# Optimization experiments

Hardware: AMD Instinct MI355X
Metric: run time of the kernel (lower is better)

## Reference

```python
import jax, jax.numpy as jnp
import numpy as np
import math

C = 512          # in_planes
H = 8            # num_heads
D = C // H       # head_dim = 64
EPS = 1e-12      # torch F.normalize eps


def _l2norm(x):
    # F.normalize(x, dim=-1): x / max(||x||_2, eps)
    n = jnp.sqrt(jnp.sum(x * x, axis=-1, keepdims=True))
    return x / jnp.maximum(n, EPS)


def setup_inputs() -> dict:
    key = jax.random.key(0)
    ks = jax.random.split(key, 8)
    q = jax.random.normal(ks[0], (8, 8, 256, C), dtype=jnp.float32)
    kv = jax.random.normal(ks[1], (8, 8, 512, C), dtype=jnp.float32)
    s = 0.02
    Wq = jax.random.normal(ks[2], (C, C), dtype=jnp.float32) * s
    bq = jax.random.normal(ks[3], (C,), dtype=jnp.float32) * s
    Wkv = jax.random.normal(ks[4], (2 * C, C), dtype=jnp.float32) * s
    bkv = jax.random.normal(ks[5], (2 * C,), dtype=jnp.float32) * s
    Wm = jax.random.normal(ks[6], (C, C), dtype=jnp.float32) * s
    bm = jax.random.normal(ks[7], (C,), dtype=jnp.float32) * s
    return {"q": q, "kv": kv, "Wq": Wq, "bq": bq, "Wkv": Wkv, "bkv": bkv, "Wm": Wm, "bm": bm}


def reference(q, kv, Wq, bq, Wkv, bkv, Wm, bm):
    b, t, lq, c = q.shape
    lk = kv.shape[2]
    shortcut = q

    # Q projection -> (b,t,h,lq,d), L2-normalized over d
    qh = (q @ Wq.T + bq).reshape(b, t, lq, H, D)
    qh = _l2norm(jnp.moveaxis(qh, 3, 2))  # (b,t,h,lq,d)

    # KV projection -> (b,t,2h,lk,d); first H heads = k, last H = v
    kvh = (kv @ Wkv.T + bkv).reshape(b, t, lk, 2 * H, D)
    kvh = jnp.moveaxis(kvh, 3, 2)          # (b,t,2h,lk,d)
    kh = _l2norm(kvh[:, :, :H])            # (b,t,h,lk,d)
    vh = _l2norm(kvh[:, :, H:])            # (b,t,h,lk,d)

    # cosine attention
    att = jnp.einsum('bthqd,bthkd->bthqk', qh, kh) / math.sqrt(D)
    att = jax.nn.softmax(att, axis=-1)
    x = jnp.einsum('bthqk,bthkd->bthqd', att, vh)  # (b,t,h,lq,d)

    # merge heads, output projection, residual
    x = jnp.moveaxis(x, 2, 3).reshape(b, t, lq, c)
    return x @ Wm.T + bm + shortcut
```

## Files before the change

### kernel.cpp

```cpp
#include <hip/hip_runtime.h>
#include <hip/hip_bf16.h>

using bf = __bf16;
typedef __attribute__((ext_vector_type(8))) __bf16 bf16x8;
typedef __attribute__((ext_vector_type(4))) float f32x4;

#define MFMA(a, b, c) __builtin_amdgcn_mfma_f32_16x16x32_bf16((a), (b), (c), 0, 0, 0)
#define GLL16(g, s)                                                         \
    __builtin_amdgcn_global_load_lds(                                       \
        (const __attribute__((address_space(1))) void*)(g),                 \
        (__attribute__((address_space(3))) void*)(s), 16, 0, 0)

static __device__ __forceinline__ void cvt_one(const float* __restrict__ s,
                                               bf* __restrict__ d, int i)
{
    const f32x4 a = ((const f32x4*)s)[2 * i];
    const f32x4 b = ((const f32x4*)s)[2 * i + 1];
    bf16x8 r;
#pragma unroll
    for (int k = 0; k < 4; ++k) { r[k] = (bf)a[k]; r[4 + k] = (bf)b[k]; }
    ((bf16x8*)d)[i] = r;
}

__global__ __launch_bounds__(256) void cvt3(const float* __restrict__ s1, bf* __restrict__ d1, int n1,
                                            const float* __restrict__ s2, bf* __restrict__ d2, int n2,
                                            const float* __restrict__ s3, bf* __restrict__ d3, int n3)
{
    int i = blockIdx.x * 256 + threadIdx.x;
    if (i < n1) { cvt_one(s1, d1, i); return; }
    i -= n1;
    if (i < n2) { cvt_one(s2, d2, i); return; }
    i -= n2;
    if (i < n3) cvt_one(s3, d3, i);
}

template <int EPI, int GH, int LGR, int AF32>
__global__ __launch_bounds__(256) void gemm128(
    const void* __restrict__ Ap, const bf* __restrict__ W,
    const float* __restrict__ bias, const float* __restrict__ res,
    void* __restrict__ Cout, int M, int N, int K)
{
    __shared__ __attribute__((aligned(16))) bf As[128 * 32];
    __shared__ __attribute__((aligned(16))) bf Bs[128 * 32];

    const int lane = threadIdx.x & 63;
    const int wave = threadIdx.x >> 6;
    const int lm = lane & 15;
    const int quad = lane >> 4;
    const int row0 = blockIdx.x * 128, col0 = blockIdx.y * 128;
    const int wrow = (wave >> 1) * 64, wcol = (wave & 1) * 64;

    const int sr = lane >> 2;
    const int sc = (lane & 3) * 8;
    const bf* Ag = nullptr;
    const float* Agf = nullptr;
    if (AF32) Agf = (const float*)Ap + (size_t)(row0 + wave * 32 + sr) * K + sc;
    else      Ag  = (const bf*)Ap + (size_t)(row0 + wave * 32 + sr) * K + sc;
    const bf* Wg = W + (size_t)(col0 + wave * 32 + sr) * K + sc;
    bf* AsW = As + wave * 1024;
    bf* BsW = Bs + wave * 1024;

    f32x4 acc[4][4] = {};

    for (int k0 = 0; k0 < K; k0 += 32) {
        if (AF32) {
            f32x4 u0 = *(const f32x4*)(Agf + k0);
            f32x4 u1 = *(const f32x4*)(Agf + k0 + 4);
            f32x4 u2 = *(const f32x4*)(Agf + (size_t)16 * K + k0);
            f32x4 u3 = *(const f32x4*)(Agf + (size_t)16 * K + k0 + 4);
            bf16x8 r0, r1;
#pragma unroll
            for (int e = 0; e < 4; ++e) {
                r0[e] = (bf)u0[e]; r0[4 + e] = (bf)u1[e];
                r1[e] = (bf)u2[e]; r1[4 + e] = (bf)u3[e];
            }
            *(bf16x8*)(AsW + lane * 8) = r0;
            *(bf16x8*)(AsW + 512 + lane * 8) = r1;
        } else {
            GLL16(Ag + k0, AsW);
            GLL16(Ag + (size_t)16 * K + k0, AsW + 512);
        }
        GLL16(Wg + k0, BsW);
        GLL16(Wg + (size_t)16 * K + k0, BsW + 512);
        __syncthreads();

        bf16x8 a[4], b[4];
#pragma unroll
        for (int i = 0; i < 4; ++i)
            a[i] = *(const bf16x8*)(As + (wrow + i * 16 + lm) * 32 + quad * 8);
#pragma unroll
        for (int j = 0; j < 4; ++j)
            b[j] = *(const bf16x8*)(Bs + (wcol + j * 16 + lm) * 32 + quad * 8);
#pragma unroll
        for (int i = 0; i < 4; ++i)
#pragma unroll
            for (int j = 0; j < 4; ++j)
                acc[i][j] = MFMA(a[i], b[j], acc[i][j]);
        __syncthreads();
    }

    float bv[4];
#pragma unroll
    for (int j = 0; j < 4; ++j) bv[j] = bias[col0 + wcol + j * 16 + lm];

    if (EPI == 0) {
        bf* C = (bf*)Cout;
        const int g = (col0 + wcol) >> 6;
#pragma unroll
        for (int i = 0; i < 4; ++i) {
#pragma unroll
            for (int rg = 0; rg < 4; ++rg) {
                float v[4];
                float ss = 0.f;
#pragma unroll
                for (int j = 0; j < 4; ++j) {
                    const float x = acc[i][j][rg] + bv[j];
                    v[j] = x;
                    ss += x * x;
                }
                ss += __shfl_xor(ss, 1, 64);
                ss += __shfl_xor(ss, 2, 64);
                ss += __shfl_xor(ss, 4, 64);
                ss += __shfl_xor(ss, 8, 64);
                const float inv = 1.0f / fmaxf(sqrtf(ss), 1e-12f);
                const int row = row0 + wrow + i * 16 + quad * 4 + rg;
                const int bt = row >> LGR;
                const int rl = row & ((1 << LGR) - 1);
                bf* Cr = C + (((size_t)(bt * GH + g) << LGR) + rl) * 64;
#pragma unroll
                for (int j = 0; j < 4; ++j)
                    Cr[j * 16 + lm] = (bf)(v[j] * inv);
            }
        }
    } else {
        float* C = (float*)Cout;
#pragma unroll
        for (int i = 0; i < 4; ++i) {
#pragma unroll
            for (int rg = 0; rg < 4; ++rg) {
                const int row = row0 + wrow + i * 16 + quad * 4 + rg;
#pragma unroll
                for (int j = 0; j < 4; ++j) {
                    const size_t idx = (size_t)row * N + col0 + wcol + j * 16 + lm;
                    C[idx] = acc[i][j][rg] + bv[j] + res[idx];
                }
            }
        }
    }
}

template <int GH, int LGR>
__global__ __launch_bounds__(512, 2) void gemm256(
    const float* __restrict__ A, const bf* __restrict__ W,
    const float* __restrict__ bias, bf* __restrict__ C,
    int M, int N, int K)
{
    extern __shared__ __attribute__((aligned(16))) char smem[];
    char* Asm = smem;
    char* Bsm = smem + 65536;

    const int tid = threadIdx.x;
    const int lane = tid & 63;
    const int lm = lane & 15;
    const int quad = lane >> 4;
    const int wave = tid >> 6;
    const int wm = wave >> 2;
    const int wn = wave & 3;
    const int row0 = blockIdx.x * 256, col0 = blockIdx.y * 256;
    const int NT = K >> 6;

    const int trow = tid >> 3;
    const int slotL = tid & 7;
    const int sphys = slotL ^ (trow & 7);
    const int tslot = slotL ^ (trow & 7);
    const float* Af = A + (size_t)(row0 + trow) * K + slotL * 8;
    const bf* Wth = W + (size_t)(col0 + trow) * K + tslot * 8;

    const char* aBase = Asm + wm * 16384 + lm * 128;
    const char* bBase = Bsm + (wn >> 1) * 16384 + ((wn & 1) * 64 + lm) * 128;
    const int skz0 = ((quad ^ (lm & 7)) << 4);
    const int skz1 = (((4 + quad) ^ (lm & 7)) << 4);

    f32x4 acc[8][4] = {};
    f32x4 areg[4][2];

    auto ldA = [&](int kt) {
#pragma unroll
        for (int hs = 0; hs < 4; ++hs) {
            const float* p = Af + (size_t)((hs >> 1) * 128 + (hs & 1) * 64) * K + kt * 64;
            areg[hs][0] = ((const f32x4*)p)[0];
            areg[hs][1] = ((const f32x4*)p)[1];
        }
    };
    auto wrA = [&](int kt) {
        const int bo = (kt & 1) * 32768;
#pragma unroll
        for (int hs = 0; hs < 4; ++hs) {
            bf16x8 r;
#pragma unroll
            for (int e = 0; e < 4; ++e) {
                r[e] = (bf)areg[hs][0][e];
                r[4 + e] = (bf)areg[hs][1][e];
            }
            *(bf16x8*)(Asm + bo + (hs >> 1) * 16384 + (hs & 1) * 8192 + trow * 128 + sphys * 16) = r;
        }
    };
    auto stB = [&](int kt) {
        const int bo = (kt & 1) * 32768;
#pragma unroll
        for (int h = 0; h < 2; ++h)
#pragma unroll
            for (int s = 0; s < 2; ++s)
                GLL16(Wth + (size_t)(h * 128 + s * 64) * K + kt * 64,
                      Bsm + bo + h * 16384 + s * 8192 + tid * 16);
    };

#define LOADA(bo, mh, kk)                                                     \
    _Pragma("unroll")                                                         \
    for (int mm = 0; mm < 4; ++mm)                                            \
        a[mm] = *(const bf16x8*)(aBase + (bo) + ((mh) * 4 + mm) * 2048        \
                                 + ((kk) ? skz1 : skz0));
#define LOADB(bo, kk)                                                         \
    _Pragma("unroll")                                                         \
    for (int j = 0; j < 4; ++j)                                               \
        b[j] = *(const bf16x8*)(bBase + (bo) + j * 2048                       \
                                + ((kk) ? skz1 : skz0));
#define PH_OPEN()                                                             \
    __builtin_amdgcn_s_barrier();                                             \
    asm volatile("s_waitcnt lgkmcnt(0)" ::: "memory");                        \
    __builtin_amdgcn_s_setprio(1)
#define MM16(mh)                                                              \
    _Pragma("unroll")                                                         \
    for (int mm = 0; mm < 4; ++mm)                                            \
        _Pragma("unroll")                                                     \
        for (int j = 0; j < 4; ++j)                                           \
            acc[(mh) * 4 + mm][j] = MFMA(a[mm], b[j], acc[(mh) * 4 + mm][j]);
#define PH_CLOSE()                                                            \
    __builtin_amdgcn_s_setprio(0);                                            \
    __builtin_amdgcn_s_barrier()

    stB(0); ldA(0); stB(1);
    asm volatile("s_waitcnt vmcnt(4)" ::: "memory");
    wrA(0);
    asm volatile("s_waitcnt lgkmcnt(0)" ::: "memory");
    __builtin_amdgcn_s_barrier();

    for (int it = 0; it < NT; it += 2) {
        const int more = (it + 2 < NT);
        bf16x8 a[4], b[4];

        LOADA(0, 0, 0) LOADB(0, 0) ldA(it + 1);
        PH_OPEN(); MM16(0) PH_CLOSE();

        LOADA(0, 1, 0)
        PH_OPEN(); MM16(1) PH_CLOSE();

        LOADA(0, 0, 1) LOADB(0, 1)
        PH_OPEN(); MM16(0) PH_CLOSE();

        LOADA(0, 1, 1) if (more) stB(it + 2);
        PH_OPEN(); MM16(1)
        __builtin_amdgcn_s_setprio(0);
        if (more) { asm volatile("s_waitcnt vmcnt(4)" ::: "memory"); }
        else      { asm volatile("s_waitcnt vmcnt(0)" ::: "memory"); }
        wrA(it + 1);
        asm volatile("s_waitcnt lgkmcnt(0)" ::: "memory");
        __builtin_amdgcn_s_barrier();

        LOADA(32768, 0, 0) LOADB(32768, 0) if (more) ldA(it + 2);
        PH_OPEN(); MM16(0) PH_CLOSE();

        LOADA(32768, 1, 0)
        PH_OPEN(); MM16(1) PH_CLOSE();

        LOADA(32768, 0, 1) LOADB(32768, 1)
        PH_OPEN(); MM16(0) PH_CLOSE();

        LOADA(32768, 1, 1) if (more) stB(it + 3);
        PH_OPEN(); MM16(1)
        __builtin_amdgcn_s_setprio(0);
        if (more) {
            asm volatile("s_waitcnt vmcnt(4)" ::: "memory");
            wrA(it + 2);
            asm volatile("s_waitcnt lgkmcnt(0)" ::: "memory");
        }
        __builtin_amdgcn_s_barrier();
    }
#undef LOADA
#undef LOADB
#undef PH_OPEN
#undef MM16
#undef PH_CLOSE

    float bv[4];
#pragma unroll
    for (int j = 0; j < 4; ++j) bv[j] = bias[col0 + wn * 64 + j * 16 + lm];
    const int g = (col0 + wn * 64) >> 6;
#pragma unroll
    for (int m = 0; m < 8; ++m) {
#pragma unroll
        for (int rg = 0; rg < 4; ++rg) {
            float v[4];
            float ss = 0.f;
#pragma unroll
            for (int j = 0; j < 4; ++j) {
                const float x = acc[m][j][rg] + bv[j];
                v[j] = x;
                ss += x * x;
            }
            ss += __shfl_xor(ss, 1, 64);
            ss += __shfl_xor(ss, 2, 64);
            ss += __shfl_xor(ss, 4, 64);
            ss += __shfl_xor(ss, 8, 64);
            const float inv = 1.0f / fmaxf(sqrtf(ss), 1e-12f);
            const int row = row0 + wm * 128 + m * 16 + quad * 4 + rg;
            const int bt = row >> LGR;
            const int rl = row & ((1 << LGR) - 1);
            bf* Cr = C + (((size_t)(bt * GH + g) << LGR) + rl) * 64;
#pragma unroll
            for (int j = 0; j < 4; ++j)
                Cr[j * 16 + lm] = (bf)(v[j] * inv);
        }
    }
}

__global__ __launch_bounds__(256, 4) void attn(
    const bf* __restrict__ qn, const bf* __restrict__ kvn, bf* __restrict__ X)
{
    __shared__ __attribute__((aligned(16))) bf Kt[128 * 72];
    __shared__ __attribute__((aligned(16))) bf Vt[64 * 136];
    __shared__ __attribute__((aligned(16))) bf Ps[4][16 * 40];

    const int qb = blockIdx.x >> 9;
    const int rb = blockIdx.x & 511;
    const int bt = rb >> 3;
    const int h = rb & 7;
    const int tid = threadIdx.x;
    const int lane = tid & 63;
    const int wave = tid >> 6;
    const int lm = lane & 15;
    const int quad = lane >> 4;

    const bf* qh = qn + ((size_t)(bt * 8 + h) * 256 + qb * 128) * 64;
    const bf* kh = kvn + (size_t)(bt * 16 + h) * 512 * 64;
    const bf* vh = kvn + (size_t)(bt * 16 + 8 + h) * 512 * 64;

    const int srow = tid >> 1;
    const int sseg = (tid & 1) * 32;

    f32x4 o[2][4] = {};
    float sum[2][4] = {};
    bf* Pw = &Ps[wave][0];

    for (int t = 0; t < 4; ++t) {
        {
            const bf* kr = kh + (size_t)(t * 128 + srow) * 64 + sseg;
            bf* kd = Kt + srow * 72 + sseg;
#pragma unroll
            for (int j = 0; j < 4; ++j)
                *(bf16x8*)(kd + j * 8) = *(const bf16x8*)(kr + j * 8);

            const bf* vr = vh + (size_t)(t * 128 + srow) * 64 + sseg;
            bf16x8 vv[4];
#pragma unroll
            for (int j = 0; j < 4; ++j) vv[j] = *(const bf16x8*)(vr + j * 8);
#pragma unroll
            for (int j = 0; j < 4; ++j)
#pragma unroll
                for (int e = 0; e < 8; ++e)
                    Vt[(sseg + j * 8 + e) * 136 + srow] = vv[j][e];
        }
        __syncthreads();

#pragma unroll
        for (int c = 0; c < 2; ++c) {
            const int r0 = wave * 32 + c * 16;
            const bf* qp = qh + (size_t)(r0 + lm) * 64 + quad * 8;
            const bf16x8 a0 = *(const bf16x8*)qp;
            const bf16x8 a1 = *(const bf16x8*)(qp + 32);

            f32x4 s[8];
#pragma unroll
            for (int nt = 0; nt < 8; ++nt) {
                const bf16x8 k0 = *(const bf16x8*)(&Kt[(nt * 16 + lm) * 72 + quad * 8]);
                const bf16x8 k1 = *(const bf16x8*)(&Kt[(nt * 16 + lm) * 72 + 32 + quad * 8]);
                f32x4 z = {};
                z = MFMA(a0, k0, z);
                s[nt] = MFMA(a1, k1, z);
            }

            for (int ntp = 0; ntp < 4; ++ntp) {
#pragma unroll
                for (int tt = 0; tt < 2; ++tt)
#pragma unroll
                    for (int rr = 0; rr < 4; ++rr) {
                        const float e = __expf(s[ntp * 2 + tt][rr] * 0.125f);
                        sum[c][rr] += e;
                        Pw[(quad * 4 + rr) * 40 + tt * 16 + lm] = (bf)e;
                    }
                const bf16x8 ap = *(const bf16x8*)(&Pw[lm * 40 + quad * 8]);
#pragma unroll
                for (int dt = 0; dt < 4; ++dt) {
                    const bf16x8 bv = *(const bf16x8*)(&Vt[(dt * 16 + lm) * 136 + ntp * 32 + quad * 8]);
                    o[c][dt] = MFMA(ap, bv, o[c][dt]);
                }
            }
        }
        __syncthreads();
    }

#pragma unroll
    for (int c = 0; c < 2; ++c) {
        float inv[4];
#pragma unroll
        for (int rr = 0; rr < 4; ++rr) {
            float sm = sum[c][rr];
            sm += __shfl_xor(sm, 1, 64);
            sm += __shfl_xor(sm, 2, 64);
            sm += __shfl_xor(sm, 4, 64);
            sm += __shfl_xor(sm, 8, 64);
            inv[rr] = 1.0f / sm;
        }
        bf* Xp = X + ((size_t)bt * 256 + qb * 128 + wave * 32 + c * 16) * 512 + h * 64;
#pragma unroll
        for (int dt = 0; dt < 4; ++dt)
#pragma unroll
            for (int rr = 0; rr < 4; ++rr)
                Xp[(size_t)(quad * 4 + rr) * 512 + dt * 16 + lm] = (bf)(o[c][dt][rr] * inv[rr]);
    }
}

extern "C" void kernel_launch(void* const* d_in, const int* in_sizes, int n_in,
                              void* d_out, int out_size, void* d_ws, size_t ws_size,
                              hipStream_t stream)
{
    const float* q   = (const float*)d_in[0];
    const float* kv  = (const float*)d_in[1];
    const float* Wq  = (const float*)d_in[2];
    const float* bq  = (const float*)d_in[3];
    const float* Wkv = (const float*)d_in[4];
    const float* bkv = (const float*)d_in[5];
    const float* Wm  = (const float*)d_in[6];
    const float* bm  = (const float*)d_in[7];
    float* out = (float*)d_out;

    char* ws = (char*)d_ws;
    bf* kvn  = (bf*)ws;
    bf* wqb  = (bf*)(ws + ((size_t)64 << 20));
    bf* wkvb = (bf*)(ws + ((size_t)64 << 20) + ((size_t)512 << 10));
    bf* wmb  = (bf*)(ws + ((size_t)65 << 20) + ((size_t)512 << 10));
    bf* X    = (bf*)(ws + ((size_t)66 << 20));
    bf* qn   = (bf*)d_out;

    {
        auto k0 = gemm256<16, 9>;
        (void)hipFuncSetAttribute((const void*)k0, hipFuncAttributeMaxDynamicSharedMemorySize, 131072);
    }

    cvt3<<<dim3(512), 256, 0, stream>>>(Wq, wqb, 32768, Wkv, wkvb, 65536, Wm, wmb, 32768);
    gemm256<16, 9><<<dim3(128, 4), 512, 131072, stream>>>(kv, wkvb, bkv, kvn, 32768, 1024, 512);
    gemm128<0, 8, 8, 1><<<dim3(128, 4), 256, 0, stream>>>(q, wqb, bq, nullptr, qn, 16384, 512, 512);
    attn<<<dim3(1024), 256, 0, stream>>>(qn, kvn, X);
    gemm128<1, 0, 0, 0><<<dim3(128, 4), 256, 0, stream>>>(X, wmb, bm, q, out, 16384, 512, 512);
}
```

Before: 295.7 us.

## Pre-convert kv to bf16 and fuse Q/KV projections into one launch

The kv activations are converted to bf16 in a separate pass, so the KV projection GEMM can stream A with direct global-to-LDS loads instead of loading fp32 into registers and converting. The Q and KV projections now run as one fused launch of 256-tile blocks, replacing the separate 128-tile Q GEMM. The Wm conversion moves into extra blocks of the attention kernel. The cost is an extra full read and write of kv in bf16, plus workspace and output-buffer aliasing that must keep lifetimes disjoint.

After: 292.7 us. About the same (-1.0%).

```diff
diff --git a/kernel.cpp b/kernel.cpp
--- a/kernel.cpp
+++ b/kernel.cpp
@@ -149,11 +149,11 @@
     }
 }
 
-template <int GH, int LGR>
-__global__ __launch_bounds__(512, 2) void gemm256(
-    const float* __restrict__ A, const bf* __restrict__ W,
+template <int GH, int LGR, int AF32>
+static __device__ __forceinline__ void gemm256_body(
+    const void* __restrict__ Ap, const bf* __restrict__ W,
     const float* __restrict__ bias, bf* __restrict__ C,
-    int M, int N, int K)
+    const int bxx, const int byy, const int K)
 {
     extern __shared__ __attribute__((aligned(16))) char smem[];
     char* Asm = smem;
@@ -166,15 +166,15 @@
     const int wave = tid >> 6;
     const int wm = wave >> 2;
     const int wn = wave & 3;
-    const int row0 = blockIdx.x * 256, col0 = blockIdx.y * 256;
+    const int row0 = bxx * 256, col0 = byy * 256;
     const int NT = K >> 6;
 
     const int trow = tid >> 3;
     const int slotL = tid & 7;
-    const int sphys = slotL ^ (trow & 7);
-    const int tslot = slotL ^ (trow & 7);
-    const float* Af = A + (size_t)(row0 + trow) * K + slotL * 8;
-    const bf* Wth = W + (size_t)(col0 + trow) * K + tslot * 8;
+    const int sswz = slotL ^ (trow & 7);
+    const float* Af = (const float*)Ap + (size_t)(row0 + trow) * K + slotL * 8;
+    const bf*    Ab = (const bf*)Ap + (size_t)(row0 + trow) * K + sswz * 8;
+    const bf*    Wth = W + (size_t)(col0 + trow) * K + sswz * 8;
 
     const char* aBase = Asm + wm * 16384 + lm * 128;
     const char* bBase = Bsm + (wn >> 1) * 16384 + ((wn & 1) * 64 + lm) * 128;
@@ -202,8 +202,17 @@
                 r[e] = (bf)areg[hs][0][e];
                 r[4 + e] = (bf)areg[hs][1][e];
             }
-            *(bf16x8*)(Asm + bo + (hs >> 1) * 16384 + (hs & 1) * 8192 + trow * 128 + sphys * 16) = r;
-        }
+            *(bf16x8*)(Asm + bo + (hs >> 1) * 16384 + (hs & 1) * 8192 + trow * 128 + sswz * 16) = r;
+        }
+    };
+    auto stAg = [&](int kt) {
+        const int bo = (kt & 1) * 32768;
+#pragma unroll
+        for (int h = 0; h < 2; ++h)
+#pragma unroll
+            for (int s = 0; s < 2; ++s)
+                GLL16(Ab + (size_t)(h * 128 + s * 64) * K + kt * 64,
+                      Asm + bo + h * 16384 + s * 8192 + tid * 16);
     };
     auto stB = [&](int kt) {
         const int bo = (kt & 1) * 32768;
@@ -239,17 +248,23 @@
     __builtin_amdgcn_s_setprio(0);                                            \
     __builtin_amdgcn_s_barrier()
 
-    stB(0); ldA(0); stB(1);
-    asm volatile("s_waitcnt vmcnt(4)" ::: "memory");
-    wrA(0);
-    asm volatile("s_waitcnt lgkmcnt(0)" ::: "memory");
+    if (AF32) {
+        stB(0); ldA(0); stB(1);
+        asm volatile("s_waitcnt vmcnt(4)" ::: "memory");
+        wrA(0);
+        asm volatile("s_waitcnt lgkmcnt(0)" ::: "memory");
+    } else {
+        stB(0); stAg(0); stB(1);
+        asm volatile("s_waitcnt vmcnt(4)" ::: "memory");
+    }
     __builtin_amdgcn_s_barrier();
 
     for (int it = 0; it < NT; it += 2) {
         const int more = (it + 2 < NT);
         bf16x8 a[4], b[4];
 
-        LOADA(0, 0, 0) LOADB(0, 0) ldA(it + 1);
+        LOADA(0, 0, 0) LOADB(0, 0)
+        if (AF32) ldA(it + 1); else stAg(it + 1);
         PH_OPEN(); MM16(0) PH_CLOSE();
 
         LOADA(0, 1, 0)
@@ -263,11 +278,14 @@
         __builtin_amdgcn_s_setprio(0);
         if (more) { asm volatile("s_waitcnt vmcnt(4)" ::: "memory"); }
         else      { asm volatile("s_waitcnt vmcnt(0)" ::: "memory"); }
-        wrA(it + 1);
-        asm volatile("s_waitcnt lgkmcnt(0)" ::: "memory");
+        if (AF32) {
+            wrA(it + 1);
+            asm volatile("s_waitcnt lgkmcnt(0)" ::: "memory");
+        }
         __builtin_amdgcn_s_barrier();
 
-        LOADA(32768, 0, 0) LOADB(32768, 0) if (more) ldA(it + 2);
+        LOADA(32768, 0, 0) LOADB(32768, 0)
+        if (more) { if (AF32) ldA(it + 2); else stAg(it + 2); }
         PH_OPEN(); MM16(0) PH_CLOSE();
 
         LOADA(32768, 1, 0)
@@ -281,8 +299,10 @@
         __builtin_amdgcn_s_setprio(0);
         if (more) {
             asm volatile("s_waitcnt vmcnt(4)" ::: "memory");
-            wrA(it + 2);
-            asm volatile("s_waitcnt lgkmcnt(0)" ::: "memory");
+            if (AF32) {
+                wrA(it + 2);
+                asm volatile("s_waitcnt lgkmcnt(0)" ::: "memory");
+            }
         }
         __builtin_amdgcn_s_barrier();
     }
@@ -324,9 +344,32 @@
     }
 }
 
+__global__ __launch_bounds__(512, 2) void fusedproj(
+    const bf* __restrict__ kvb, const bf* __restrict__ wkvb,
+    const float* __restrict__ bkv, bf* __restrict__ kvn,
+    const float* __restrict__ q, const bf* __restrict__ wqb,
+    const float* __restrict__ bq, bf* __restrict__ qn)
+{
+    const int bx = blockIdx.x;
+    if (bx < 128) {
+        gemm256_body<8, 8, 1>((const void*)q, wqb, bq, qn, bx & 63, bx >> 6, 512);
+    } else {
+        const int b2 = bx - 128;
+        gemm256_body<16, 9, 0>((const void*)kvb, wkvb, bkv, kvn, b2 & 127, b2 >> 7, 512);
+    }
+}
+
 __global__ __launch_bounds__(256, 4) void attn(
-    const bf* __restrict__ qn, const bf* __restrict__ kvn, bf* __restrict__ X)
-{
+    const bf* __restrict__ qn, const bf* __restrict__ kvn, bf* __restrict__ X,
+    const float* __restrict__ Wm, bf* __restrict__ wmb)
+{
+    if (blockIdx.x >= 1024) {
+        const int t = (blockIdx.x - 1024) * 256 + threadIdx.x;
+#pragma unroll 4
+        for (int u = t; u < 32768; u += 1024) cvt_one(Wm, wmb, u);
+        return;
+    }
+
     __shared__ __attribute__((aligned(16))) bf Kt[128 * 72];
     __shared__ __attribute__((aligned(16))) bf Vt[64 * 136];
     __shared__ __attribute__((aligned(16))) bf Ps[4][16 * 40];
@@ -445,21 +488,20 @@
     float* out = (float*)d_out;
 
     char* ws = (char*)d_ws;
-    bf* kvn  = (bf*)ws;
-    bf* wqb  = (bf*)(ws + ((size_t)64 << 20));
-    bf* wkvb = (bf*)(ws + ((size_t)64 << 20) + ((size_t)512 << 10));
-    bf* wmb  = (bf*)(ws + ((size_t)65 << 20) + ((size_t)512 << 10));
-    bf* X    = (bf*)(ws + ((size_t)66 << 20));
-    bf* qn   = (bf*)d_out;
-
-    {
-        auto k0 = gemm256<16, 9>;
-        (void)hipFuncSetAttribute((const void*)k0, hipFuncAttributeMaxDynamicSharedMemorySize, 131072);
-    }
-
-    cvt3<<<dim3(512), 256, 0, stream>>>(Wq, wqb, 32768, Wkv, wkvb, 65536, Wm, wmb, 32768);
-    gemm256<16, 9><<<dim3(128, 4), 512, 131072, stream>>>(kv, wkvb, bkv, kvn, 32768, 1024, 512);
-    gemm128<0, 8, 8, 1><<<dim3(128, 4), 256, 0, stream>>>(q, wqb, bq, nullptr, qn, 16384, 512, 512);
-    attn<<<dim3(1024), 256, 0, stream>>>(qn, kvn, X);
+    bf* kvb = (bf*)ws;
+    bf* kvn = (bf*)(ws + ((size_t)32 << 20));
+    bf* X   = (bf*)ws;
+    bf* wmb = (bf*)(ws + ((size_t)16 << 20));
+    char* dob = (char*)d_out;
+    bf* wkvb = (bf*)dob;
+    bf* wqb  = (bf*)(dob + ((size_t)1 << 20));
+    bf* qn   = (bf*)(dob + ((size_t)16 << 20));
+
+    (void)hipFuncSetAttribute((const void*)fusedproj,
+                              hipFuncAttributeMaxDynamicSharedMemorySize, 131072);
+
+    cvt3<<<dim3(8576), 256, 0, stream>>>(kv, kvb, 2097152, Wkv, wkvb, 65536, Wq, wqb, 32768);
+    fusedproj<<<dim3(640), 512, 131072, stream>>>(kvb, wkvb, bkv, kvn, q, wqb, bq, qn);
+    attn<<<dim3(1028), 256, 0, stream>>>(qn, kvn, X, Wm, wmb);
     gemm128<1, 0, 0, 0><<<dim3(128, 4), 256, 0, stream>>>(X, wmb, bm, q, out, 16384, 512, 512);
 }
```
